# Kernel tuning notes

Measured on AMD Instinct MI355X. Metric: run time of the kernel, lower is better.

The kernel has to match this reference:

```python
import jax, jax.numpy as jnp
import numpy as np
from jax import lax

S = 224          # raster_settings.image_size
K = 10           # raster_settings.faces_per_pixel
BLUR = 1e-4      # raster_settings.blur_radius (signed squared-dist threshold)
SIGMA = 1e-4     # BlendParams().sigma used by sigmoid_alpha_blend
BIG = 1e10
AREA_EPS = 1e-10


def setup_inputs():
    key = jax.random.key(0)
    k1, k2, k3 = jax.random.split(key, 3)
    B, V, F = 2, 5023, 5000
    xy = jax.random.uniform(k1, (B, V, 2), minval=-1.0, maxval=1.0)
    z = jax.random.uniform(k2, (B, V, 1), minval=0.5, maxval=1.5)
    vertices = jnp.concatenate([xy, z], -1).astype(jnp.float32)
    faces = jax.random.randint(k3, (B, F, 3), 0, V, dtype=jnp.int32)
    return {"vertices": vertices, "faces": faces}


def _cross2(a, b):
    return a[..., 0] * b[..., 1] - a[..., 1] * b[..., 0]


def _edge_d2(a, b, p):
    # squared distance from points p [W,1,2] to segment (a,b) [F,2] -> [W,F]
    ab = b - a
    ap = p - a
    t = jnp.clip((ap * ab).sum(-1) / jnp.maximum((ab * ab).sum(-1), 1e-12), 0.0, 1.0)
    proj = a + t[..., None] * ab
    return ((p - proj) ** 2).sum(-1)


def _rasterize_one(verts, faces):
    # naive PyTorch3D-style rasterizer for one mesh: per pixel, keep K nearest
    # faces (by interpolated z) whose signed squared dist to the triangle < BLUR.
    tri = verts[faces]                                  # [F,3,3]
    v0, v1, v2 = tri[:, 0, :2], tri[:, 1, :2], tri[:, 2, :2]
    z0, z1, z2 = tri[:, 0, 2], tri[:, 1, 2], tri[:, 2, 2]
    area = _cross2(v1 - v0, v2 - v0)
    good_face = jnp.abs(area) > AREA_EPS                # cull degenerate faces
    area_safe = jnp.where(good_face, area, 1.0)
    # NDC pixel centers (pytorch3d convention: +x left, +y up; verts pre-negated)
    coords = 1.0 - (2.0 * jnp.arange(S, dtype=verts.dtype) + 1.0) / S

    def row(yf):
        p = jnp.stack([coords, jnp.full((S,), yf, verts.dtype)], -1)[:, None, :]  # [W,1,2]
        w0 = _cross2(v2 - v1, p - v1) / area_safe       # [W,F] barycentric
        w1 = _cross2(v0 - v2, p - v2) / area_safe
        w2 = _cross2(v1 - v0, p - v0) / area_safe
        z = w0 * z0 + w1 * z1 + w2 * z2                  # no perspective correction (default)
        inside = (w0 > 0) & (w1 > 0) & (w2 > 0)
        d2 = jnp.minimum(jnp.minimum(_edge_d2(v0, v1, p), _edge_d2(v1, v2, p)),
                         _edge_d2(v2, v0, p))
        sd = jnp.where(inside, -d2, d2)                  # signed squared dist
        valid = good_face & (z > 0) & (sd <= BLUR)
        negz = jnp.where(valid, -z, -BIG)
        vals, idx = lax.top_k(negz, K)                   # K nearest by z
        vk = vals > -0.5 * BIG
        zk = jnp.take_along_axis(z, idx, -1)
        dk = jnp.take_along_axis(sd, idx, -1)
        return (jnp.where(vk, idx, -1), jnp.where(vk, zk, -1.0), jnp.where(vk, dk, -1.0))

    return lax.map(row, coords)                          # each [S,S,K]


def reference(vertices, faces):
    B, V, _ = vertices.shape
    F = faces.shape[1]
    fixed = vertices * jnp.array([-1.0, -1.0, 1.0], vertices.dtype)  # flip x,y (DECA)
    p2f_l, zbuf, dists = jax.vmap(_rasterize_one)(fixed, faces)      # [B,S,S,K]
    mask = p2f_l >= 0
    # packed (global) pix_to_face like pytorch3d
    p2f = jnp.where(mask, p2f_l + (jnp.arange(B) * F)[:, None, None, None], -1)
    # sigmoid_alpha_blend: alpha = 1 - prod(1 - sigmoid(-dist/sigma))
    prob = jax.nn.sigmoid(-dists / SIGMA) * mask
    alpha = 1.0 - jnp.prod(1.0 - prob, -1)               # [B,S,S]
    images = alpha[:, None, :, :]                        # images[...,3:].permute(0,3,1,2)
    # vertex visibility from nearest face per pixel (scatter)
    faces_packed = (faces + V * jnp.arange(B, dtype=faces.dtype)[:, None, None]).reshape(-1, 3)
    faces_all = jnp.concatenate([faces_packed, -jnp.ones((1, 3), faces.dtype)], 0)
    vis_verts = faces_all[p2f[..., 0].reshape(-1)].reshape(-1)  # -1 wraps to sentinel row
    vv = jnp.zeros(B * V + 1, vertices.dtype).at[vis_verts].set(1.0)
    visibility = vv[:-1].reshape(B, V)                   # extra slot absorbs -1 indices
    return images, visibility
```

## Files before the change

### kernel.cpp

```cpp
#include <hip/hip_runtime.h>
#include <math.h>

#define SDIM 224
#define KTOP 10
#define NB 2
#define NV 5023
#define NF 5000
#define BLUR 1e-4f
#define IMG_SZ (NB * SDIM * SDIM)
#define NW 8
#define SEG (NF / NW)
#define CAP 1024
#define Q1 20
#define HT 0.031251f
#define COV_THR 0.04422f
#define REL_THR (-0.0543f)

__device__ __forceinline__ float seg_d2_exact(float ax, float ay, float abx, float aby,
                                              float L, float px, float py) {
    float apx = __fsub_rn(px, ax), apy = __fsub_rn(py, ay);
    float dot = __fadd_rn(__fmul_rn(apx, abx), __fmul_rn(apy, aby));
    float t = __fdiv_rn(dot, L);
    t = fminf(fmaxf(t, 0.0f), 1.0f);
    float prx = __fadd_rn(ax, __fmul_rn(t, abx));
    float pry = __fadd_rn(ay, __fmul_rn(t, aby));
    float dx = __fsub_rn(px, prx), dy = __fsub_rn(py, pry);
    return __fadd_rn(__fmul_rn(dx, dx), __fmul_rn(dy, dy));
}

__global__ void preprocess_kernel(const float* __restrict__ verts,
                                  const int* __restrict__ faces,
                                  float4* __restrict__ ga,
                                  float4* __restrict__ hh,
                                  float4* __restrict__ cc,
                                  float* __restrict__ out)
{
    const int idx = blockIdx.x * blockDim.x + threadIdx.x;
    if (idx < NB * NV) out[IMG_SZ + idx] = 0.0f;
    if (idx >= NB * NF) return;
    const int b = idx / NF;
    const int* fp = faces + (size_t)idx * 3;
    const int i0 = fp[0], i1 = fp[1], i2 = fp[2];
    const float* vb = verts + (size_t)b * NV * 3;
    const float v0x = -vb[i0*3+0], v0y = -vb[i0*3+1], z0 = vb[i0*3+2];
    const float v1x = -vb[i1*3+0], v1y = -vb[i1*3+1], z1 = vb[i1*3+2];
    const float v2x = -vb[i2*3+0], v2y = -vb[i2*3+1], z2 = vb[i2*3+2];
    const float e01x = __fsub_rn(v1x, v0x), e01y = __fsub_rn(v1y, v0y);
    const float e12x = __fsub_rn(v2x, v1x), e12y = __fsub_rn(v2y, v1y);
    const float e20x = __fsub_rn(v0x, v2x), e20y = __fsub_rn(v0y, v2y);
    const float area = __fsub_rn(__fmul_rn(e01x, __fsub_rn(v2y, v0y)),
                                 __fmul_rn(e01y, __fsub_rn(v2x, v0x)));
    const bool good = fabsf(area) > 1e-10f;
    const float area_safe = good ? area : 1.0f;

    double Zx = 0.0, Zy = 0.0, Zc = 0.0;
    float mgc = -1.0f;
    float n0x=0,n0y=0,n0c=-3e38f, n1x=0,n1y=0,n1c=-3e38f, n2x=0,n2y=0,n2c=-3e38f;
    float zloF = 3e38f, zhiF = -1.0f;
    if (good) {
        const double invA = 1.0 / (double)area;
        const double c0c = (double)e12y*v1x - (double)e12x*v1y;
        const double c1c = (double)e20y*v2x - (double)e20x*v2y;
        const double c2c = (double)e01y*v0x - (double)e01x*v0y;
        Zx = (-(double)e12y*z0 - (double)e20y*z1 - (double)e01y*z2) * invA;
        Zy = ( (double)e12x*z0 + (double)e20x*z1 + (double)e01x*z2) * invA;
        Zc = (c0c*z0 + c1c*z1 + c2c*z2) * invA;
        const double B0 = fabs((double)e12x)*(1.0+fabs((double)v1y)) + fabs((double)e12y)*(1.0+fabs((double)v1x));
        const double B1 = fabs((double)e20x)*(1.0+fabs((double)v2y)) + fabs((double)e20y)*(1.0+fabs((double)v2x));
        const double B2 = fabs((double)e01x)*(1.0+fabs((double)v0y)) + fabs((double)e01y)*(1.0+fabs((double)v0x));
        const double B = (B0*(double)z0 + B1*(double)z1 + B2*(double)z2) * fabs(invA);
        mgc = (float)(2.5e-6 * B) + 1e-20f;
        const double s = (area > 0.0f) ? 1.0 : -1.0;
        const double l12 = sqrt((double)e12x*e12x + (double)e12y*e12y);
        const double l20 = sqrt((double)e20x*e20x + (double)e20y*e20y);
        const double l01 = sqrt((double)e01x*e01x + (double)e01y*e01y);
        const double i12 = s / fmax(l12, 1e-300);
        const double i20 = s / fmax(l20, 1e-300);
        const double i01 = s / fmax(l01, 1e-300);
        n0x = (float)(-(double)e12y * i12);
        n0y = (float)( (double)e12x * i12);
        n0c = (float)(((double)e12y*v1x - (double)e12x*v1y) * i12);
        n1x = (float)(-(double)e20y * i20);
        n1y = (float)( (double)e20x * i20);
        n1c = (float)(((double)e20y*v2x - (double)e20x*v2y) * i20);
        n2x = (float)(-(double)e01y * i01);
        n2y = (float)( (double)e01x * i01);
        n2c = (float)(((double)e01y*v0x - (double)e01x*v0y) * i01);
        const double gradZ = sqrt(Zx*Zx + Zy*Zy);
        const double zminV = fmin((double)z0, fmin((double)z1, (double)z2));
        const double zmaxV = fmax((double)z0, fmax((double)z1, (double)z2));
        zloF = (float)(zminV - 0.0102 * gradZ - (double)mgc - 1e-6);
        const bool elig = (zminV - (double)mgc - 1e-6) > 0.0;
        zhiF = elig ? (float)(zmaxV + (double)mgc + 1e-6) : -1.0f;
    }
    ga[idx]     = make_float4((float)Zx, (float)Zy, (float)Zc, mgc);
    cc[3*idx+0] = make_float4(n0x, n0y, n0c, n1x);
    cc[3*idx+1] = make_float4(n1y, n1c, n2x, n2y);
    cc[3*idx+2] = make_float4(n2c, zloF, zhiF, 0.0f);
    hh[3*idx+0] = make_float4(v0x, v0y, v1x, v1y);
    hh[3*idx+1] = make_float4(v2x, v2y, z0, z1);
    hh[3*idx+2] = make_float4(z2, area_safe, 0.0f, 0.0f);
}

__device__ __forceinline__ void heavy_face(float4 h0, float4 h1, float4 h2,
                                           int fidx, bool pass, float px, float py,
                                           float tz[KTOP], float ts[KTOP],
                                           float& bestZ, int& bestIdx)
{
    if (!pass) return;
    const float v0x=h0.x, v0y=h0.y, v1x=h0.z, v1y=h0.w;
    const float v2x=h1.x, v2y=h1.y, z0=h1.z, z1=h1.w;
    const float z2=h2.x, area=h2.y;
    const float e01x = __fsub_rn(v1x, v0x), e01y = __fsub_rn(v1y, v0y);
    const float e12x = __fsub_rn(v2x, v1x), e12y = __fsub_rn(v2y, v1y);
    const float e20x = __fsub_rn(v0x, v2x), e20y = __fsub_rn(v0y, v2y);

    const float c0 = __fsub_rn(__fmul_rn(e12x, __fsub_rn(py, v1y)),
                               __fmul_rn(e12y, __fsub_rn(px, v1x)));
    const float c1 = __fsub_rn(__fmul_rn(e20x, __fsub_rn(py, v2y)),
                               __fmul_rn(e20y, __fsub_rn(px, v2x)));
    const float c2 = __fsub_rn(__fmul_rn(e01x, __fsub_rn(py, v0y)),
                               __fmul_rn(e01y, __fsub_rn(px, v0x)));

    const float L01 = fmaxf(__fadd_rn(__fmul_rn(e01x,e01x), __fmul_rn(e01y,e01y)), 1e-12f);
    const float L12 = fmaxf(__fadd_rn(__fmul_rn(e12x,e12x), __fmul_rn(e12y,e12y)), 1e-12f);
    const float L20 = fmaxf(__fadd_rn(__fmul_rn(e20x,e20x), __fmul_rn(e20y,e20y)), 1e-12f);

    const bool ap = area > 0.0f;
    const bool s0 = ap ? (c0 > 0.0f) : (c0 < 0.0f);
    const bool s1 = ap ? (c1 > 0.0f) : (c1 < 0.0f);
    const bool s2 = ap ? (c2 > 0.0f) : (c2 < 0.0f);
    if (!(s0 & s1 & s2)) {
        bool cull = false;
        if (!s0) cull |= (c0 * c0 > BLUR * 1.0002f * L12);
        if (!s1) cull |= (c1 * c1 > BLUR * 1.0002f * L20);
        if (!s2) cull |= (c2 * c2 > BLUR * 1.0002f * L01);
        if (cull) return;
    }

    const float w0 = __fdiv_rn(c0, area);
    const float w1 = __fdiv_rn(c1, area);
    const float w2 = __fdiv_rn(c2, area);
    const float z = __fadd_rn(__fadd_rn(__fmul_rn(w0, z0), __fmul_rn(w1, z1)),
                              __fmul_rn(w2, z2));
    if (!(z > 0.0f)) return;
    if (!(z < tz[KTOP-1])) return;

    const bool inside = (w0 > 0.0f) & (w1 > 0.0f) & (w2 > 0.0f);
    float sd;
    if (inside) {
        const bool sat = (c0*c0 >= 1.0002e-3f * L12) &
                         (c1*c1 >= 1.0002e-3f * L20) &
                         (c2*c2 >= 1.0002e-3f * L01);
        if (sat) {
            sd = -1.0f;
        } else {
            const float d2 = fminf(fminf(
                seg_d2_exact(v0x, v0y, e01x, e01y, L01, px, py),
                seg_d2_exact(v1x, v1y, e12x, e12y, L12, px, py)),
                seg_d2_exact(v2x, v2y, e20x, e20y, L20, px, py));
            sd = -d2;
        }
    } else {
        const float d2 = fminf(fminf(
            seg_d2_exact(v0x, v0y, e01x, e01y, L01, px, py),
            seg_d2_exact(v1x, v1y, e12x, e12y, L12, px, py)),
            seg_d2_exact(v2x, v2y, e20x, e20y, L20, px, py));
        if (!(d2 <= BLUR)) return;
        sd = d2;
    }

    if (z < bestZ) { bestZ = z; bestIdx = fidx; }

    float cz = z, cs = sd;
#pragma unroll
    for (int j = 0; j < KTOP; ++j) {
        if (cz < tz[j]) {
            const float oz = tz[j], os = ts[j];
            tz[j] = cz; ts[j] = cs; cz = oz; cs = os;
        }
    }
}

__global__ __launch_bounds__(64 * NW, 6) void raster_kernel(const float4* __restrict__ gaG,
                                                            const float4* __restrict__ hhG,
                                                            const float4* __restrict__ ccG,
                                                            const int* __restrict__ faces,
                                                            float* __restrict__ out)
{
    const int b = blockIdx.z;
    const int lane = threadIdx.x & 63;
    const int w = __builtin_amdgcn_readfirstlane((int)(threadIdx.x >> 6));
    const int x = (blockIdx.x << 3) + (lane & 7);
    const int y = (blockIdx.y << 3) + (lane >> 3);
    const float px = __fsub_rn(1.0f, __fdiv_rn(__fadd_rn(__fmul_rn(2.0f, (float)x), 1.0f), (float)SDIM));
    const float py = __fsub_rn(1.0f, __fdiv_rn(__fadd_rn(__fmul_rn(2.0f, (float)y), 1.0f), (float)SDIM));
    const float pcx = __fsub_rn(1.0f, __fdiv_rn((float)(16 * blockIdx.x + 8), 224.0f));
    const float pcy = __fsub_rn(1.0f, __fdiv_rn((float)(16 * blockIdx.y + 8), 224.0f));

    __shared__ int   sList[CAP];
    __shared__ unsigned short sQ[NW * Q1 * 64];
    __shared__ int   sHist[64];
    __shared__ int   sCnt[NW];
    __shared__ int   sOff[NW];
    __shared__ int   sLen;
    __shared__ int   sOvf;
    __shared__ float sT;
    __shared__ float sZ[NW][64][11];
    __shared__ float sS[NW][64][11];
    __shared__ int   sBI[NW][64];

    if (threadIdx.x < 64) sHist[threadIdx.x] = 0;
    if (threadIdx.x == 0) sOvf = 0;
    __syncthreads();

    const float4* __restrict__ ga = gaG + (size_t)b * NF;
    const float4* __restrict__ hh = hhG + (size_t)b * NF * 3;
    const float4* __restrict__ cc = ccG + (size_t)b * NF * 3;

    const int f0 = w * SEG, f1 = f0 + SEG;
    float dm[10], zl[10];
#pragma unroll
    for (int it = 0; it < 10; ++it) {
        const int f = f0 + it * 64 + lane;
        dm[it] = -3e38f; zl[it] = 3e38f;
        if (f < f1) {
            const float4 a0 = ga[f];
            const float4 cA = cc[3*f+0];
            const float4 cB = cc[3*f+1];
            const float4 cC = cc[3*f+2];
            const float d0 = fmaf(cA.x, pcx, fmaf(cA.y, pcy, cA.z));
            const float d1 = fmaf(cA.w, pcx, fmaf(cB.x, pcy, cB.y));
            const float d2 = fmaf(cB.z, pcx, fmaf(cB.w, pcy, cC.x));
            const float dmin = fminf(d0, fminf(d1, d2));
            const float ztc = fmaf(a0.x, pcx, fmaf(a0.y, pcy, a0.z));
            const float spread = fmaf(fabsf(a0.x), HT, fmaf(fabsf(a0.y), HT, 2.0f * fabsf(a0.w))) + 1e-6f;
            dm[it] = dmin;
            zl[it] = fmaxf(ztc - spread, cC.y);
            if ((cC.z > 0.0f) && (dmin >= COV_THR)) {
                const float zh = fminf(ztc + spread, cC.z);
                int bk = (int)floorf((zh - 0.4f) * 53.333332f);
                bk = max(0, min(63, bk));
                atomicAdd(&sHist[bk], 1);
            }
        }
    }
    __syncthreads();

    if (threadIdx.x == 0) {
        int cum = 0; float T = 3e38f;
        for (int k2 = 0; k2 < 64; ++k2) {
            cum += sHist[k2];
            if (cum >= KTOP) { T = (k2 >= 63) ? 3e38f : (0.4f + (float)(k2+1) * 0.01875f + 1e-4f); break; }
        }
        sT = T;
    }
    __syncthreads();
    const float Tt = sT;

    int svMask = 0, cnt1 = 0;
#pragma unroll
    for (int it = 0; it < 10; ++it) {
        const bool sv = (dm[it] >= REL_THR) && (zl[it] <= Tt);
        if (sv) svMask |= (1 << it);
        cnt1 += (int)__popcll(__ballot(sv));
    }
    if (lane == 0) sCnt[w] = cnt1;
    __syncthreads();
    if (threadIdx.x == 0) {
        int acc = 0;
        for (int w2 = 0; w2 < NW; ++w2) { sOff[w2] = acc; acc += sCnt[w2]; }
        sLen = (acc <= CAP) ? acc : -1;
    }
    __syncthreads();
    const int Ltot = sLen;

    if (Ltot >= 0) {
        const unsigned long long below = ((lane == 63) ? ~0ull : ((1ull << (lane + 1)) - 1ull)) >> 1;
        int woff = sOff[w];
#pragma unroll
        for (int it = 0; it < 10; ++it) {
            const bool sv = (svMask >> it) & 1;
            const unsigned long long m = __ballot(sv);
            if (sv) sList[woff + (int)__popcll(m & below)] = f0 + it * 64 + lane;
            woff += (int)__popcll(m);
        }
    }
    __syncthreads();

    float tz[KTOP], ts[KTOP];
#pragma unroll
    for (int j = 0; j < KTOP; ++j) { tz[j] = 3e38f; ts[j] = 3e38f; }
    float bestZ = 3e38f;
    int bestIdx = -1;

    int qn = 0;
    int jb = 0, je = 0;
    if (Ltot >= 0) {
        const int chunk = (Ltot + NW - 1) / NW;
        jb = w * chunk; je = min(Ltot, jb + chunk);
        for (int j = jb; j < je; ++j) {
            const int f = __builtin_amdgcn_readfirstlane(sList[j]);
            const float4 g = ga[f];
            const float4 cA = cc[3*f+0];
            const float4 cB = cc[3*f+1];
            const float4 cC = cc[3*f+2];
            const float zt = fmaf(g.x, px, fmaf(g.y, py, g.z));
            const float d0 = fmaf(cA.x, px, fmaf(cA.y, py, cA.z));
            const float d1 = fmaf(cA.w, px, fmaf(cB.x, py, cB.y));
            const float d2 = fmaf(cB.z, px, fmaf(cB.w, py, cC.x));
            const float dmin = fminf(d0, fminf(d1, d2));
            const bool pass = (zt > -g.w) & (zt < Tt + g.w) & (dmin >= -0.0102f);
            if (pass) {
                if (qn < Q1) { sQ[(w * Q1 + qn) * 64 + lane] = (unsigned short)f; qn++; }
                else atomicOr(&sOvf, 1);
            }
        }
    }
    __syncthreads();
    const int ovf = sOvf;

    if (Ltot >= 0 && !ovf) {
        for (int i = 0; __any(i < qn); ++i) {
            const bool act = (i < qn);
            const int f = act ? (int)sQ[(w * Q1 + i) * 64 + lane] : 0;
            const float4 h0 = hh[3*f+0];
            const float4 h1 = hh[3*f+1];
            const float4 h2 = hh[3*f+2];
            heavy_face(h0, h1, h2, f, act, px, py, tz, ts, bestZ, bestIdx);
        }
    } else if (Ltot >= 0) {
        for (int j = jb; j < je; ++j) {
            const int f = __builtin_amdgcn_readfirstlane(sList[j]);
            const float4 g = ga[f];
            const float zt  = fmaf(g.x, px, fmaf(g.y, py, g.z));
            const float thr = fminf(tz[KTOP-1], Tt);
            const bool pass = (zt > -g.w) & (zt < thr + g.w);
            if (__any(pass)) {
                heavy_face(hh[3*f+0], hh[3*f+1], hh[3*f+2], f, pass, px, py,
                           tz, ts, bestZ, bestIdx);
            }
        }
    } else {
        for (int f = f0; f < f1; ++f) {
            const float4 g = ga[f];
            const float zt  = fmaf(g.x, px, fmaf(g.y, py, g.z));
            const float thr = fminf(tz[KTOP-1], Tt);
            const bool pass = (zt > -g.w) & (zt < thr + g.w);
            if (__any(pass)) {
                heavy_face(hh[3*f+0], hh[3*f+1], hh[3*f+2], f, pass, px, py,
                           tz, ts, bestZ, bestIdx);
            }
        }
    }

#pragma unroll
    for (int j = 0; j < KTOP; ++j) { sZ[w][lane][j] = tz[j]; sS[w][lane][j] = ts[j]; }
    sZ[w][lane][KTOP] = 3e38f;
    sBI[w][lane] = bestIdx;
    __syncthreads();

    if (threadIdx.x < 64) {
        const int p = threadIdx.x;
        float bz = sZ[0][p][0]; int bi = sBI[0][p];
#pragma unroll
        for (int w2 = 1; w2 < NW; ++w2) {
            const float zc = sZ[w2][p][0];
            if (zc < bz) { bz = zc; bi = sBI[w2][p]; }
        }
        int ptr[NW];
#pragma unroll
        for (int w2 = 0; w2 < NW; ++w2) ptr[w2] = 0;
        float prod = 1.0f;
#pragma unroll
        for (int k = 0; k < KTOP; ++k) {
            float mz = 3e38f; int mw = -1;
#pragma unroll
            for (int w2 = 0; w2 < NW; ++w2) {
                const float zc = sZ[w2][p][ptr[w2]];
                if (zc < mz) { mz = zc; mw = w2; }
            }
            float sd = 3e38f;
#pragma unroll
            for (int w2 = 0; w2 < NW; ++w2) {
                if (w2 == mw) { sd = sS[w2][p][ptr[w2]]; ptr[w2]++; }
            }
            prod *= 1.0f / (1.0f + __expf(-sd * 1e4f));
        }
        const float alpha = 1.0f - prod;
        const int gx = (blockIdx.x << 3) + (p & 7);
        const int gy = (blockIdx.y << 3) + (p >> 3);
        out[(size_t)b * (SDIM * SDIM) + gy * SDIM + gx] = alpha;

        if (bi >= 0) {
            const int* fp = faces + ((size_t)b * NF + bi) * 3;
            float* vis = out + IMG_SZ;
            vis[b * NV + fp[0]] = 1.0f;
            vis[b * NV + fp[1]] = 1.0f;
            vis[b * NV + fp[2]] = 1.0f;
        }
    }
}

extern "C" void kernel_launch(void* const* d_in, const int* in_sizes, int n_in,
                              void* d_out, int out_size, void* d_ws, size_t ws_size,
                              hipStream_t stream)
{
    const float* verts = (const float*)d_in[0];
    const int*   faces = (const int*)d_in[1];
    float* out = (float*)d_out;
    float4* ga = (float4*)d_ws;
    float4* hh = (float4*)((char*)d_ws + NB * NF * 16);
    float4* cc = (float4*)((char*)d_ws + NB * NF * (16 + 48));

    const int total = NB * NV;
    preprocess_kernel<<<dim3((total + 255) / 256), dim3(256), 0, stream>>>(verts, faces, ga, hh, cc, out);
    raster_kernel<<<dim3(SDIM / 8, SDIM / 8, NB), dim3(64 * NW), 0, stream>>>(ga, hh, cc, faces, out);
}
```

Before: 190.9 us.

## Flush per-wave candidate queue incrementally and store blend distances in fp16

```diff
diff --git a/kernel.cpp b/kernel.cpp
--- a/kernel.cpp
+++ b/kernel.cpp
@@ -1,4 +1,5 @@
 #include <hip/hip_runtime.h>
+#include <hip/hip_fp16.h>
 #include <math.h>
 
 #define SDIM 224
@@ -11,7 +12,7 @@
 #define NW 8
 #define SEG (NF / NW)
 #define CAP 1024
-#define Q1 20
+#define Q1 12
 #define HT 0.031251f
 #define COV_THR 0.04422f
 #define REL_THR (-0.0543f)
@@ -204,14 +205,12 @@
     __shared__ int   sCnt[NW];
     __shared__ int   sOff[NW];
     __shared__ int   sLen;
-    __shared__ int   sOvf;
     __shared__ float sT;
-    __shared__ float sZ[NW][64][11];
-    __shared__ float sS[NW][64][11];
+    __shared__ float  sZ[NW][64][11];
+    __shared__ __half sS[NW][64][KTOP];
     __shared__ int   sBI[NW][64];
 
     if (threadIdx.x < 64) sHist[threadIdx.x] = 0;
-    if (threadIdx.x == 0) sOvf = 0;
     __syncthreads();
 
     const float4* __restrict__ ga = gaG + (size_t)b * NF;
@@ -294,11 +293,11 @@
     float bestZ = 3e38f;
     int bestIdx = -1;
 
-    int qn = 0;
-    int jb = 0, je = 0;
     if (Ltot >= 0) {
         const int chunk = (Ltot + NW - 1) / NW;
-        jb = w * chunk; je = min(Ltot, jb + chunk);
+        const int jb = w * chunk, je = min(Ltot, jb + chunk);
+        int qn = 0;
+        float thr = Tt;
         for (int j = jb; j < je; ++j) {
             const int f = __builtin_amdgcn_readfirstlane(sList[j]);
             const float4 g = ga[f];
@@ -310,36 +309,28 @@
             const float d1 = fmaf(cA.w, px, fmaf(cB.x, py, cB.y));
             const float d2 = fmaf(cB.z, px, fmaf(cB.w, py, cC.x));
             const float dmin = fminf(d0, fminf(d1, d2));
-            const bool pass = (zt > -g.w) & (zt < Tt + g.w) & (dmin >= -0.0102f);
-            if (pass) {
-                if (qn < Q1) { sQ[(w * Q1 + qn) * 64 + lane] = (unsigned short)f; qn++; }
-                else atomicOr(&sOvf, 1);
+            const bool pass = (zt > -g.w) & (zt < thr + g.w) & (dmin >= -0.0102f);
+            if (pass) { sQ[(w * Q1 + qn) * 64 + lane] = (unsigned short)f; qn++; }
+            if (__any(qn == Q1)) {
+                for (int i = 0; __any(i < qn); ++i) {
+                    const bool act = (i < qn);
+                    const int fq = act ? (int)sQ[(w * Q1 + i) * 64 + lane] : 0;
+                    const float4 h0 = hh[3*fq+0];
+                    const float4 h1 = hh[3*fq+1];
+                    const float4 h2 = hh[3*fq+2];
+                    heavy_face(h0, h1, h2, fq, act, px, py, tz, ts, bestZ, bestIdx);
+                }
+                qn = 0;
+                thr = fminf(Tt, tz[KTOP-1]);
             }
         }
-    }
-    __syncthreads();
-    const int ovf = sOvf;
-
-    if (Ltot >= 0 && !ovf) {
         for (int i = 0; __any(i < qn); ++i) {
             const bool act = (i < qn);
-            const int f = act ? (int)sQ[(w * Q1 + i) * 64 + lane] : 0;
-            const float4 h0 = hh[3*f+0];
-            const float4 h1 = hh[3*f+1];
-            const float4 h2 = hh[3*f+2];
-            heavy_face(h0, h1, h2, f, act, px, py, tz, ts, bestZ, bestIdx);
-        }
-    } else if (Ltot >= 0) {
-        for (int j = jb; j < je; ++j) {
-            const int f = __builtin_amdgcn_readfirstlane(sList[j]);
-            const float4 g = ga[f];
-            const float zt  = fmaf(g.x, px, fmaf(g.y, py, g.z));
-            const float thr = fminf(tz[KTOP-1], Tt);
-            const bool pass = (zt > -g.w) & (zt < thr + g.w);
-            if (__any(pass)) {
-                heavy_face(hh[3*f+0], hh[3*f+1], hh[3*f+2], f, pass, px, py,
-                           tz, ts, bestZ, bestIdx);
-            }
+            const int fq = act ? (int)sQ[(w * Q1 + i) * 64 + lane] : 0;
+            const float4 h0 = hh[3*fq+0];
+            const float4 h1 = hh[3*fq+1];
+            const float4 h2 = hh[3*fq+2];
+            heavy_face(h0, h1, h2, fq, act, px, py, tz, ts, bestZ, bestIdx);
         }
     } else {
         for (int f = f0; f < f1; ++f) {
@@ -355,7 +346,10 @@
     }
 
 #pragma unroll
-    for (int j = 0; j < KTOP; ++j) { sZ[w][lane][j] = tz[j]; sS[w][lane][j] = ts[j]; }
+    for (int j = 0; j < KTOP; ++j) {
+        sZ[w][lane][j] = tz[j];
+        sS[w][lane][j] = __float2half(ts[j]);
+    }
     sZ[w][lane][KTOP] = 3e38f;
     sBI[w][lane] = bestIdx;
     __syncthreads();
@@ -383,7 +377,7 @@
             float sd = 3e38f;
 #pragma unroll
             for (int w2 = 0; w2 < NW; ++w2) {
-                if (w2 == mw) { sd = sS[w2][p][ptr[w2]]; ptr[w2]++; }
+                if (w2 == mw) { sd = __half2float(sS[w2][p][ptr[w2]]); ptr[w2]++; }
             }
             prod *= 1.0f / (1.0f + __expf(-sd * 1e4f));
         }
```

After: 201.0 us. 5.3% more time.
